# Performance work log

Hardware: AMD Instinct MI355X
Metric: run time of the kernel (lower is better)

## Reference

```python
import jax, jax.numpy as jnp
import numpy as np

BN_EPS = 1e-5


def setup_inputs() -> dict:
    key = jax.random.key(0)
    k1, k2, k3 = jax.random.split(key, 3)
    n, d = 4096, 128
    x = jax.random.normal(k1, (2 * n, d), dtype=jnp.float32)
    affinity_A = jax.random.normal(k2, (n, n), dtype=jnp.float32)
    # Xavier-uniform-like init for the [d, d] weight
    lim = float(np.sqrt(6.0 / (d + d)))
    weight = jax.random.uniform(k3, (d, d), dtype=jnp.float32, minval=-lim, maxval=lim)
    gamma = jnp.ones((d,), dtype=jnp.float32)
    beta = jnp.zeros((d,), dtype=jnp.float32)
    return {"x": x, "affinity_A": affinity_A, "weight": weight, "gamma": gamma, "beta": beta}


def reference(x, affinity_A, weight, gamma, beta):
    # Binarize affinity
    A = jnp.where(affinity_A > 0, 1.0, 0.0).astype(x.dtype)  # [n, n]
    n = A.shape[0]
    I = jnp.eye(n, dtype=x.dtype)
    # Block adjacency [[A, I], [I, A]] -> [2n, 2n]
    adj = jnp.block([[A, I], [I, A]])
    # Symmetric normalization D^{-1/2} A D^{-1/2}.
    # (Original code materializes D^{-1/2} as a full matrix and does two O(n^3)
    # matmuls; mathematically it is just row/column scaling, done here directly.)
    deg = adj.sum(axis=1)                 # [2n], >= 1 because of identity blocks
    dinv = deg ** -0.5
    norm_A = dinv[:, None] * adj * dinv[None, :]
    # GCN propagation: (norm_A @ x) @ W
    h = (norm_A @ x) @ weight             # [2n, d]
    # BatchNorm1d (training mode, biased variance) + ReLU
    mean = h.mean(axis=0)
    var = h.var(axis=0)
    h = (h - mean) * jax.lax.rsqrt(var + BN_EPS) * gamma + beta
    return jax.nn.relu(h)
```

## Files before the change

### kernel.cpp

```cpp
#include <hip/hip_runtime.h>
#include <stdint.h>


#define N_NODES 4096
#define D 128
#define TWO_N (2*N_NODES)

typedef unsigned short u16;
typedef unsigned int u32;
typedef __bf16 bf16;
typedef bf16 bf16x8 __attribute__((ext_vector_type(8)));
typedef float f32x4 __attribute__((ext_vector_type(4)));
typedef u16 u16x8 __attribute__((ext_vector_type(8)));

__device__ __forceinline__ float bf2f(u16 u) {
    return __builtin_bit_cast(float, ((unsigned)u) << 16);
}
__device__ __forceinline__ u16 f2bf(float f) {
    unsigned b = __builtin_bit_cast(unsigned, f);
    unsigned r = (b + 0x7FFFu + ((b >> 16) & 1u)) >> 16;
    return (u16)r;
}
__device__ __forceinline__ bool det_fp32(const u16* gamma) {
    return gamma[0] != (u16)0x3F80;
}

__global__ void k_degscale(const void* __restrict__ x, const void* __restrict__ aff,
                           const void* __restrict__ W, const u16* __restrict__ gamma,
                           float* __restrict__ dinv, u16* __restrict__ XsT,
                           u16* __restrict__ WT, unsigned char* __restrict__ Abits) {
    int t = threadIdx.x;
    bool fp32 = det_fp32(gamma);
    const u16* W16 = (const u16*)W;
    const float* W32 = (const float*)W;

    if (blockIdx.x >= 512) {
        int b = blockIdx.x - 512;
        int ol = t >> 4;
        int o = b * 16 + ol;
        int cg = (t & 15) * 8;
        u16x8 wv;
        #pragma unroll
        for (int e = 0; e < 8; ++e) {
            size_t wi = (size_t)(cg + e) * D + o;
            float v = fp32 ? W32[wi] : bf2f(W16[wi]);
            wv[e] = f2bf(v);
        }
        int ks = cg >> 5, qc = (cg >> 3) & 3;
        *reinterpret_cast<u16x8*>(WT + (size_t)((ks * 8 + b) * 64 + qc * 16 + ol) * 8) = wv;
        return;
    }

    __shared__ int scnt[8];
    __shared__ float sdinv[8];
    int wid = t >> 6, lane = t & 63;
    int j0 = blockIdx.x * 8;

    int cnt[2] = {0, 0};
    if (!fp32) {
        const u16* base = (const u16*)aff + (size_t)(j0 + wid * 2) * N_NODES;
        #pragma unroll
        for (int r = 0; r < 2; ++r) {
            unsigned char* ab = Abits + (size_t)(j0 + wid * 2 + r) * 512 + lane;
            #pragma unroll
            for (int it = 0; it < 8; ++it) {
                u16x8 v = *reinterpret_cast<const u16x8*>(base + (size_t)r * N_NODES + it * 512 + lane * 8);
                unsigned bb = 0;
                #pragma unroll
                for (int e = 0; e < 8; ++e) bb |= ((short)v[e] > 0) ? (1u << e) : 0u;
                cnt[r] += __builtin_popcount(bb);
                ab[it * 64] = (unsigned char)bb;
            }
        }
    } else {
        const float* base = (const float*)aff + (size_t)(j0 + wid * 2) * N_NODES;
        #pragma unroll
        for (int r = 0; r < 2; ++r) {
            unsigned char* ab = Abits + (size_t)(j0 + wid * 2 + r) * 512 + lane;
            #pragma unroll
            for (int it = 0; it < 8; ++it) {
                f32x4 va = *reinterpret_cast<const f32x4*>(base + (size_t)r * N_NODES + it * 512 + lane * 8);
                f32x4 vb = *reinterpret_cast<const f32x4*>(base + (size_t)r * N_NODES + it * 512 + lane * 8 + 4);
                unsigned bb = 0;
                #pragma unroll
                for (int e = 0; e < 4; ++e) {
                    bb |= (va[e] > 0.f) ? (1u << e) : 0u;
                    bb |= (vb[e] > 0.f) ? (1u << (4 + e)) : 0u;
                }
                cnt[r] += __builtin_popcount(bb);
                ab[it * 64] = (unsigned char)bb;
            }
        }
    }
    #pragma unroll
    for (int r = 0; r < 2; ++r) {
        int c = cnt[r];
        #pragma unroll
        for (int off = 32; off; off >>= 1) c += __shfl_down(c, off, 64);
        if (lane == 0) scnt[wid * 2 + r] = c;
    }
    __syncthreads();
    if (t < 8) {
        float d = rsqrtf((float)(scnt[t] + 1));
        sdinv[t] = d;
        dinv[j0 + t] = d;
    }
    __syncthreads();

    int cc = t & 127;
    const u16* xb16 = (const u16*)x + ((t < 128) ? (size_t)0 : (size_t)N_NODES * D);
    const float* xb32 = (const float*)x + ((t < 128) ? (size_t)0 : (size_t)N_NODES * D);
    u16x8 b0;
    #pragma unroll
    for (int jl = 0; jl < 8; ++jl) {
        size_t xi = (size_t)(j0 + jl) * D + cc;
        float xv = fp32 ? xb32[xi] : bf2f(xb16[xi]);
        b0[jl] = f2bf(sdinv[jl] * xv);
    }
    int kb = j0 >> 5, qd = (j0 >> 3) & 3, cg = t >> 4, r15 = t & 15;
    *reinterpret_cast<u16x8*>(XsT + (((size_t)kb * 16 + cg) * 64 + qd * 16 + r15) * 8) = b0;
}

#define SK 4
#define KCHUNK (N_NODES / SK)
#define LDA 72

#define PREFB(KK, PBV)                                                              \
    {                                                                               \
        _Pragma("unroll")                                                           \
        for (int ks = 0; ks < 2; ++ks) {                                            \
            _Pragma("unroll")                                                       \
            for (int j = 0; j < 4; ++j)                                             \
                PBV[ks * 4 + j] = *reinterpret_cast<const u16x8*>(                  \
                    pB0 + ((KK) * 2 + ks) * 8192 + j * 512);                        \
        }                                                                           \
    }

#define MFMA_PHASE(BUF, PBV)                                                        \
    {                                                                               \
        _Pragma("unroll")                                                           \
        for (int ks = 0; ks < 2; ++ks) {                                            \
            bf16x8 af[4];                                                           \
            _Pragma("unroll")                                                       \
            for (int i = 0; i < 4; ++i)                                             \
                af[i] = *reinterpret_cast<const bf16x8*>(                           \
                    &sA[BUF][(i * 16 + l15) * LDA + ks * 32 + quad * 8]);           \
            _Pragma("unroll")                                                       \
            for (int j = 0; j < 4; ++j) {                                           \
                bf16x8 bfr = __builtin_bit_cast(bf16x8, PBV[ks * 4 + j]);           \
                _Pragma("unroll")                                                   \
                for (int i = 0; i < 4; ++i)                                         \
                    acc[i][j] = __builtin_amdgcn_mfma_f32_16x16x32_bf16(            \
                        af[i], bfr, acc[i][j], 0, 0, 0);                            \
            }                                                                       \
        }                                                                           \
    }

__launch_bounds__(256, 1)
__global__ void k_gemm(const unsigned char* __restrict__ Abits, const u16* __restrict__ XsT,
                       u16* __restrict__ Ypart) {
    __shared__ unsigned char sBits[64 * 128];
    __shared__ u16 sA[2][64 * LDA];
    int tid = threadIdx.x;
    int mt = blockIdx.x >> 2;
    int sk = blockIdx.x & 3;
    int rm0 = mt * 64;
    int lane = tid & 63, wid = tid >> 6;
    int quad = lane >> 4, l15 = lane & 15;

    f32x4 acc[4][4];
    #pragma unroll
    for (int i = 0; i < 4; ++i)
        #pragma unroll
        for (int j = 0; j < 4; ++j) acc[i][j] = (f32x4){0.f, 0.f, 0.f, 0.f};

    {
        int r = tid >> 2, seg = tid & 3;
        const unsigned char* g = Abits + (size_t)(rm0 + r) * 512 + sk * 128 + seg * 32;
        u16x8 lo = *reinterpret_cast<const u16x8*>(g);
        u16x8 hi = *reinterpret_cast<const u16x8*>(g + 16);
        int swz = (r & 7) << 4;
        *reinterpret_cast<u16x8*>(sBits + r * 128 + ((seg * 32) ^ swz)) = lo;
        *reinterpret_cast<u16x8*>(sBits + r * 128 + ((seg * 32 + 16) ^ swz)) = hi;
    }

    int er = tid & 63, eq = tid >> 6;
    int eswz = (er & 7) << 4;
    auto expand = [&](int kk, int buf) {
        u16 w = *reinterpret_cast<const u16*>(sBits + er * 128 + (((kk << 3) + eq * 2) ^ eswz));
        u32 out[8];
        #pragma unroll
        for (int m = 0; m < 8; ++m)
            out[m] = ((w >> (2 * m)) & 1u) * 0x3F80u
                   | (u32)((w >> (2 * m + 1)) & 1u) * 0x3F800000u;
        *reinterpret_cast<u16x8*>(&sA[buf][er * LDA + eq * 16]) =
            *reinterpret_cast<u16x8*>(&out[0]);
        *reinterpret_cast<u16x8*>(&sA[buf][er * LDA + eq * 16 + 8]) =
            *reinterpret_cast<u16x8*>(&out[4]);
    };

    const u16* pB0 = XsT + (((size_t)sk * 512 + wid * 4) * 64 + lane) * 8;

    u16x8 pbA[8], pbB[8];
    __syncthreads();
    expand(0, 0);
    PREFB(0, pbA);

    for (int kk = 0; kk < 16; kk += 2) {
        __syncthreads();
        PREFB(kk + 1, pbB);
        expand(kk + 1, 1);
        MFMA_PHASE(0, pbA);
        __syncthreads();
        if (kk + 2 < 16) {
            PREFB(kk + 2, pbA);
            expand(kk + 2, 0);
        }
        MFMA_PHASE(1, pbB);
    }

    u16* yp = Ypart + (size_t)sk * N_NODES * 256;
    #pragma unroll
    for (int i = 0; i < 4; ++i) {
        int row = rm0 + i * 16 + quad * 4;
        #pragma unroll
        for (int j = 0; j < 4; ++j) {
            int col = wid * 64 + j * 16 + l15;
            #pragma unroll
            for (int r = 0; r < 4; ++r)
                yp[(size_t)(row + r) * 256 + col] = f2bf(acc[i][j][r]);
        }
    }
}

__global__ void k_comb(const u16* __restrict__ Ypart, const void* __restrict__ x,
                       const u16* __restrict__ WT, const u16* __restrict__ gamma,
                       const float* __restrict__ dinv, u16* __restrict__ hpre,
                       float* __restrict__ pS, float* __restrict__ pQ) {
    __shared__ u16 sH[32 * 136];
    __shared__ float sOut[32 * 132];
    int t = threadIdx.x;
    bool fp32 = det_fp32(gamma);
    int r0 = blockIdx.x * 32;
    bool top = blockIdx.x < 128;
    int node0 = top ? r0 : r0 - N_NODES;
    const u16* x16 = (const u16*)x;
    const float* x32 = (const float*)x;

    int lane = t & 63, wid = t >> 6;
    int wm = wid >> 1, wn = wid & 1;
    int quad = lane >> 4, l15 = lane & 15;

    u16x8 wf[4][4];
    #pragma unroll
    for (int ks = 0; ks < 4; ++ks)
        #pragma unroll
        for (int j = 0; j < 4; ++j)
            wf[ks][j] = *reinterpret_cast<const u16x8*>(
                WT + (size_t)((ks * 8 + wn * 4 + j) * 64 + lane) * 8);

    #pragma unroll
    for (int p = 0; p < 2; ++p) {
        int r = (t >> 4) + p * 16;
        int c0 = (t & 15) * 8;
        int node = node0 + r;
        int ycol = (top ? 0 : 128) + c0;
        float fs[8] = {0.f, 0.f, 0.f, 0.f, 0.f, 0.f, 0.f, 0.f};
        #pragma unroll
        for (int sk = 0; sk < SK; ++sk) {
            u16x8 yv = *reinterpret_cast<const u16x8*>(Ypart + ((size_t)sk * N_NODES + node) * 256 + ycol);
            #pragma unroll
            for (int e = 0; e < 8; ++e) fs[e] += bf2f(yv[e]);
        }
        float dv = dinv[node];
        size_t xi = (top ? (size_t)(N_NODES + node) : (size_t)node) * D + c0;
        u16x8 hv;
        if (!fp32) {
            u16x8 xv = *reinterpret_cast<const u16x8*>(x16 + xi);
            #pragma unroll
            for (int e = 0; e < 8; ++e) hv[e] = f2bf(dv * fs[e] + dv * dv * bf2f(xv[e]));
        } else {
            f32x4 xa = *reinterpret_cast<const f32x4*>(x32 + xi);
            f32x4 xb = *reinterpret_cast<const f32x4*>(x32 + xi + 4);
            #pragma unroll
            for (int e = 0; e < 4; ++e) {
                hv[e]     = f2bf(dv * fs[e]     + dv * dv * xa[e]);
                hv[4 + e] = f2bf(dv * fs[4 + e] + dv * dv * xb[e]);
            }
        }
        *reinterpret_cast<u16x8*>(sH + r * 136 + c0) = hv;
    }
    __syncthreads();

    f32x4 acc[4];
    #pragma unroll
    for (int j = 0; j < 4; ++j) acc[j] = (f32x4){0.f, 0.f, 0.f, 0.f};
    #pragma unroll
    for (int ks = 0; ks < 4; ++ks) {
        bf16x8 af = *reinterpret_cast<const bf16x8*>(sH + (wm * 16 + l15) * 136 + ks * 32 + quad * 8);
        #pragma unroll
        for (int j = 0; j < 4; ++j) {
            bf16x8 bfr = __builtin_bit_cast(bf16x8, wf[ks][j]);
            acc[j] = __builtin_amdgcn_mfma_f32_16x16x32_bf16(af, bfr, acc[j], 0, 0, 0);
        }
    }
    #pragma unroll
    for (int j = 0; j < 4; ++j) {
        int row = wm * 16 + quad * 4;
        int col = wn * 64 + j * 16 + l15;
        #pragma unroll
        for (int r = 0; r < 4; ++r) sOut[(row + r) * 132 + col] = acc[j][r];
    }
    __syncthreads();
    #pragma unroll
    for (int p = 0; p < 16; ++p) {
        int idx = p * 256 + t;
        int r = idx >> 7, c = idx & 127;
        hpre[(size_t)(r0 + r) * D + c] = f2bf(sOut[r * 132 + c]);
    }
    if (t < 128) {
        float s = 0.f, q = 0.f;
        #pragma unroll
        for (int r = 0; r < 32; ++r) {
            float v = sOut[r * 132 + t];
            s += v; q += v * v;
        }
        pS[blockIdx.x * 128 + t] = s;
        pQ[blockIdx.x * 128 + t] = q;
    }
}

__global__ void k_stats(const float* __restrict__ pS, const float* __restrict__ pQ,
                        const void* __restrict__ gamma, const void* __restrict__ beta,
                        const u16* __restrict__ gdet, float* __restrict__ scsh) {
    __shared__ float rs[256], rq[256];
    int t = threadIdx.x;
    int c0 = blockIdx.x * 8;
    int cl = t & 7;
    int rr = t >> 3;
    float s = 0.f, q = 0.f;
    #pragma unroll
    for (int i = 0; i < 8; ++i) {
        int row = rr + i * 32;
        s += pS[row * 128 + c0 + cl];
        q += pQ[row * 128 + c0 + cl];
    }
    rs[t] = s; rq[t] = q;
    __syncthreads();
    #pragma unroll
    for (int st = 128; st >= 8; st >>= 1) {
        if (t < st) { rs[t] += rs[t + st]; rq[t] += rq[t + st]; }
        __syncthreads();
    }
    if (t < 8) {
        bool fp32 = det_fp32(gdet);
        int c = c0 + t;
        float mean = rs[t] * (1.0f / TWO_N);
        float var = fmaxf(rq[t] * (1.0f / TWO_N) - mean * mean, 0.f);
        float inv = rsqrtf(var + 1e-5f);
        float g = fp32 ? ((const float*)gamma)[c] : bf2f(((const u16*)gamma)[c]);
        float b = fp32 ? ((const float*)beta)[c]  : bf2f(((const u16*)beta)[c]);
        scsh[c] = inv * g;
        scsh[128 + c] = b - mean * inv * g;
    }
}

__global__ void k_bn(const u16* __restrict__ hpre, const float* __restrict__ scsh,
                     const u16* __restrict__ gdet, void* __restrict__ out) {
    __shared__ float ssc[128], ssh[128];
    int t = threadIdx.x;
    bool fp32 = det_fp32(gdet);
    if (t < 128) { ssc[t] = scsh[t]; ssh[t] = scsh[128 + t]; }
    __syncthreads();
    size_t base = (size_t)blockIdx.x * 2048 + t * 8;
    int c0 = (t & 15) * 8;
    u16x8 hv = *reinterpret_cast<const u16x8*>(hpre + base);
    if (!fp32) {
        u16x8 ov;
        #pragma unroll
        for (int e = 0; e < 8; ++e) {
            float v = bf2f(hv[e]) * ssc[c0 + e] + ssh[c0 + e];
            ov[e] = f2bf(fmaxf(v, 0.f));
        }
        *reinterpret_cast<u16x8*>((u16*)out + base) = ov;
    } else {
        float* o = (float*)out + base;
        #pragma unroll
        for (int e = 0; e < 8; ++e) {
            float v = bf2f(hv[e]) * ssc[c0 + e] + ssh[c0 + e];
            o[e] = fmaxf(v, 0.f);
        }
    }
}

extern "C" void kernel_launch(void* const* d_in, const int* in_sizes, int n_in,
                              void* d_out, int out_size, void* d_ws, size_t ws_size,
                              hipStream_t stream) {
    const void* x = d_in[0];
    const void* aff = d_in[1];
    const void* W = d_in[2];
    const u16* gamma = (const u16*)d_in[3];
    const void* beta = d_in[4];

    char* ws = (char*)d_ws;
    u16* XsT = (u16*)ws;
    u16* hpre = XsT;
    u16* Ypart = (u16*)(ws + 2097152);
    float* dinv = (float*)(ws + 10485760);
    float* pS = (float*)(ws + 10502144);
    float* pQ = (float*)(ws + 10633216);
    float* scsh = (float*)(ws + 10764288);
    u16* WT = (u16*)(ws + 10765312);
    unsigned char* Abits = (unsigned char*)(ws + 10798080);

    k_degscale<<<520, 256, 0, stream>>>(x, aff, W, gamma, dinv, XsT, WT, Abits);
    k_gemm<<<256, 256, 0, stream>>>(Abits, XsT, Ypart);
    k_comb<<<256, 256, 0, stream>>>(Ypart, x, WT, gamma, dinv, hpre, pS, pQ);
    k_stats<<<16, 256, 0, stream>>>(pS, pQ, gamma, beta, gamma, scsh);
    k_bn<<<512, 256, 0, stream>>>(hpre, scsh, gamma, d_out);
}
```

Before: 131.3 us.

## Fold BN stats kernel into atomics and halve rows per degree-scale block

Removes the separate k_stats launch. k_comb now atomically accumulates per-column sums and sums of squares into global buffers, which are zeroed inside k_degscale. k_bn computes the scale and shift itself from those totals. Separately, k_degscale now handles 4 rows per block instead of 8 and launches twice as many blocks, which gives more parallelism for the affinity binarization; in exchange its XsT writes become half-width (4 bf16 values instead of 8). The atomics make the float summation order nondeterministic and add contention on 256 addresses.

```diff
diff --git a/kernel.cpp b/kernel.cpp
--- a/kernel.cpp
+++ b/kernel.cpp
@@ -12,6 +12,7 @@
 typedef bf16 bf16x8 __attribute__((ext_vector_type(8)));
 typedef float f32x4 __attribute__((ext_vector_type(4)));
 typedef u16 u16x8 __attribute__((ext_vector_type(8)));
+typedef u16 u16x4 __attribute__((ext_vector_type(4)));
 
 __device__ __forceinline__ float bf2f(u16 u) {
     return __builtin_bit_cast(float, ((unsigned)u) << 16);
@@ -28,14 +29,19 @@
 __global__ void k_degscale(const void* __restrict__ x, const void* __restrict__ aff,
                            const void* __restrict__ W, const u16* __restrict__ gamma,
                            float* __restrict__ dinv, u16* __restrict__ XsT,
-                           u16* __restrict__ WT, unsigned char* __restrict__ Abits) {
+                           u16* __restrict__ WT, unsigned char* __restrict__ Abits,
+                           float* __restrict__ gS, float* __restrict__ gQ) {
     int t = threadIdx.x;
     bool fp32 = det_fp32(gamma);
     const u16* W16 = (const u16*)W;
     const float* W32 = (const float*)W;
 
-    if (blockIdx.x >= 512) {
-        int b = blockIdx.x - 512;
+    if (blockIdx.x >= 1024) {
+        int b = blockIdx.x - 1024;
+        if (b == 0) {
+            if (t < 128) gS[t] = 0.f;
+            else if (t < 256) gQ[t - 128] = 0.f;
+        }
         int ol = t >> 4;
         int o = b * 16 + ol;
         int cg = (t & 15) * 8;
@@ -51,56 +57,48 @@
         return;
     }
 
-    __shared__ int scnt[8];
-    __shared__ float sdinv[8];
+    __shared__ int scnt[4];
+    __shared__ float sdinv[4];
     int wid = t >> 6, lane = t & 63;
-    int j0 = blockIdx.x * 8;
-
-    int cnt[2] = {0, 0};
-    if (!fp32) {
-        const u16* base = (const u16*)aff + (size_t)(j0 + wid * 2) * N_NODES;
-        #pragma unroll
-        for (int r = 0; r < 2; ++r) {
-            unsigned char* ab = Abits + (size_t)(j0 + wid * 2 + r) * 512 + lane;
+    int j0 = blockIdx.x * 4;
+
+    int cnt = 0;
+    {
+        int row = j0 + wid;
+        unsigned char* ab = Abits + (size_t)row * 512 + lane;
+        if (!fp32) {
+            const u16* base = (const u16*)aff + (size_t)row * N_NODES;
             #pragma unroll
             for (int it = 0; it < 8; ++it) {
-                u16x8 v = *reinterpret_cast<const u16x8*>(base + (size_t)r * N_NODES + it * 512 + lane * 8);
+                u16x8 v = *reinterpret_cast<const u16x8*>(base + it * 512 + lane * 8);
                 unsigned bb = 0;
                 #pragma unroll
                 for (int e = 0; e < 8; ++e) bb |= ((short)v[e] > 0) ? (1u << e) : 0u;
-                cnt[r] += __builtin_popcount(bb);
+                cnt += __builtin_popcount(bb);
                 ab[it * 64] = (unsigned char)bb;
             }
-        }
-    } else {
-        const float* base = (const float*)aff + (size_t)(j0 + wid * 2) * N_NODES;
-        #pragma unroll
-        for (int r = 0; r < 2; ++r) {
-            unsigned char* ab = Abits + (size_t)(j0 + wid * 2 + r) * 512 + lane;
+        } else {
+            const float* base = (const float*)aff + (size_t)row * N_NODES;
             #pragma unroll
             for (int it = 0; it < 8; ++it) {
-                f32x4 va = *reinterpret_cast<const f32x4*>(base + (size_t)r * N_NODES + it * 512 + lane * 8);
-                f32x4 vb = *reinterpret_cast<const f32x4*>(base + (size_t)r * N_NODES + it * 512 + lane * 8 + 4);
+                f32x4 va = *reinterpret_cast<const f32x4*>(base + it * 512 + lane * 8);
+                f32x4 vb = *reinterpret_cast<const f32x4*>(base + it * 512 + lane * 8 + 4);
                 unsigned bb = 0;
                 #pragma unroll
                 for (int e = 0; e < 4; ++e) {
                     bb |= (va[e] > 0.f) ? (1u << e) : 0u;
                     bb |= (vb[e] > 0.f) ? (1u << (4 + e)) : 0u;
                 }
-                cnt[r] += __builtin_popcount(bb);
+                cnt += __builtin_popcount(bb);
                 ab[it * 64] = (unsigned char)bb;
             }
         }
     }
     #pragma unroll
-    for (int r = 0; r < 2; ++r) {
-        int c = cnt[r];
-        #pragma unroll
-        for (int off = 32; off; off >>= 1) c += __shfl_down(c, off, 64);
-        if (lane == 0) scnt[wid * 2 + r] = c;
-    }
-    __syncthreads();
-    if (t < 8) {
+    for (int off = 32; off; off >>= 1) cnt += __shfl_down(cnt, off, 64);
+    if (lane == 0) scnt[wid] = cnt;
+    __syncthreads();
+    if (t < 4) {
         float d = rsqrtf((float)(scnt[t] + 1));
         sdinv[t] = d;
         dinv[j0 + t] = d;
@@ -110,15 +108,16 @@
     int cc = t & 127;
     const u16* xb16 = (const u16*)x + ((t < 128) ? (size_t)0 : (size_t)N_NODES * D);
     const float* xb32 = (const float*)x + ((t < 128) ? (size_t)0 : (size_t)N_NODES * D);
-    u16x8 b0;
-    #pragma unroll
-    for (int jl = 0; jl < 8; ++jl) {
+    u16x4 b0;
+    #pragma unroll
+    for (int jl = 0; jl < 4; ++jl) {
         size_t xi = (size_t)(j0 + jl) * D + cc;
         float xv = fp32 ? xb32[xi] : bf2f(xb16[xi]);
         b0[jl] = f2bf(sdinv[jl] * xv);
     }
     int kb = j0 >> 5, qd = (j0 >> 3) & 3, cg = t >> 4, r15 = t & 15;
-    *reinterpret_cast<u16x8*>(XsT + (((size_t)kb * 16 + cg) * 64 + qd * 16 + r15) * 8) = b0;
+    size_t ei = (((size_t)kb * 16 + cg) * 64 + qd * 16 + r15) * 8 + (j0 & 7);
+    *reinterpret_cast<u16x4*>(XsT + ei) = b0;
 }
 
 #define SK 4
@@ -236,7 +235,7 @@
 __global__ void k_comb(const u16* __restrict__ Ypart, const void* __restrict__ x,
                        const u16* __restrict__ WT, const u16* __restrict__ gamma,
                        const float* __restrict__ dinv, u16* __restrict__ hpre,
-                       float* __restrict__ pS, float* __restrict__ pQ) {
+                       float* __restrict__ gS, float* __restrict__ gQ) {
     __shared__ u16 sH[32 * 136];
     __shared__ float sOut[32 * 132];
     int t = threadIdx.x;
@@ -325,52 +324,27 @@
             float v = sOut[r * 132 + t];
             s += v; q += v * v;
         }
-        pS[blockIdx.x * 128 + t] = s;
-        pQ[blockIdx.x * 128 + t] = q;
-    }
-}
-
-__global__ void k_stats(const float* __restrict__ pS, const float* __restrict__ pQ,
-                        const void* __restrict__ gamma, const void* __restrict__ beta,
-                        const u16* __restrict__ gdet, float* __restrict__ scsh) {
-    __shared__ float rs[256], rq[256];
-    int t = threadIdx.x;
-    int c0 = blockIdx.x * 8;
-    int cl = t & 7;
-    int rr = t >> 3;
-    float s = 0.f, q = 0.f;
-    #pragma unroll
-    for (int i = 0; i < 8; ++i) {
-        int row = rr + i * 32;
-        s += pS[row * 128 + c0 + cl];
-        q += pQ[row * 128 + c0 + cl];
-    }
-    rs[t] = s; rq[t] = q;
-    __syncthreads();
-    #pragma unroll
-    for (int st = 128; st >= 8; st >>= 1) {
-        if (t < st) { rs[t] += rs[t + st]; rq[t] += rq[t + st]; }
-        __syncthreads();
-    }
-    if (t < 8) {
-        bool fp32 = det_fp32(gdet);
-        int c = c0 + t;
-        float mean = rs[t] * (1.0f / TWO_N);
-        float var = fmaxf(rq[t] * (1.0f / TWO_N) - mean * mean, 0.f);
-        float inv = rsqrtf(var + 1e-5f);
-        float g = fp32 ? ((const float*)gamma)[c] : bf2f(((const u16*)gamma)[c]);
-        float b = fp32 ? ((const float*)beta)[c]  : bf2f(((const u16*)beta)[c]);
-        scsh[c] = inv * g;
-        scsh[128 + c] = b - mean * inv * g;
-    }
-}
-
-__global__ void k_bn(const u16* __restrict__ hpre, const float* __restrict__ scsh,
-                     const u16* __restrict__ gdet, void* __restrict__ out) {
+        atomicAdd(&gS[t], s);
+        atomicAdd(&gQ[t], q);
+    }
+}
+
+__global__ void k_bn(const u16* __restrict__ hpre, const float* __restrict__ gS,
+                     const float* __restrict__ gQ, const void* __restrict__ gamma,
+                     const void* __restrict__ beta, const u16* __restrict__ gdet,
+                     void* __restrict__ out) {
     __shared__ float ssc[128], ssh[128];
     int t = threadIdx.x;
     bool fp32 = det_fp32(gdet);
-    if (t < 128) { ssc[t] = scsh[t]; ssh[t] = scsh[128 + t]; }
+    if (t < 128) {
+        float mean = gS[t] * (1.0f / TWO_N);
+        float var = fmaxf(gQ[t] * (1.0f / TWO_N) - mean * mean, 0.f);
+        float inv = rsqrtf(var + 1e-5f);
+        float g = fp32 ? ((const float*)gamma)[t] : bf2f(((const u16*)gamma)[t]);
+        float b = fp32 ? ((const float*)beta)[t]  : bf2f(((const u16*)beta)[t]);
+        ssc[t] = inv * g;
+        ssh[t] = b - mean * inv * g;
+    }
     __syncthreads();
     size_t base = (size_t)blockIdx.x * 2048 + t * 8;
     int c0 = (t & 15) * 8;
@@ -407,15 +381,13 @@
     u16* hpre = XsT;
     u16* Ypart = (u16*)(ws + 2097152);
     float* dinv = (float*)(ws + 10485760);
-    float* pS = (float*)(ws + 10502144);
-    float* pQ = (float*)(ws + 10633216);
-    float* scsh = (float*)(ws + 10764288);
+    float* gS = (float*)(ws + 10502144);
+    float* gQ = (float*)(ws + 10502656);
     u16* WT = (u16*)(ws + 10765312);
     unsigned char* Abits = (unsigned char*)(ws + 10798080);
 
-    k_degscale<<<520, 256, 0, stream>>>(x, aff, W, gamma, dinv, XsT, WT, Abits);
+    k_degscale<<<1032, 256, 0, stream>>>(x, aff, W, gamma, dinv, XsT, WT, Abits, gS, gQ);
     k_gemm<<<256, 256, 0, stream>>>(Abits, XsT, Ypart);
-    k_comb<<<256, 256, 0, stream>>>(Ypart, x, WT, gamma, dinv, hpre, pS, pQ);
-    k_stats<<<16, 256, 0, stream>>>(pS, pQ, gamma, beta, gamma, scsh);
-    k_bn<<<512, 256, 0, stream>>>(hpre, scsh, gamma, d_out);
-}
+    k_comb<<<256, 256, 0, stream>>>(Ypart, x, WT, gamma, dinv, hpre, gS, gQ);
+    k_bn<<<512, 256, 0, stream>>>(hpre, gS, gQ, gamma, beta, gamma, d_out);
+}
```

After: 134.5 us. 1.02x slower.
